# Kernel tuning notes

Measured on AMD Instinct MI355X. Metric: run time of the kernel, lower is better.

Reference implementation:

```python
import jax, jax.numpy as jnp
import numpy as np

# ranges from init_kwargs
T2P_RANGE = (1.0, 500.0)
B1_RANGE = (0.2, 1.6)

NX, NY = 256, 256
NUM_T2S, NUM_B1S, ETL = 100, 30, 16


def _nan_to_num0(x):
    # torch.nan_to_num(x, nan=0.0, posinf=0.0); inputs here are non-negative so
    # neginf never occurs, but we zero it too for safety.
    return jnp.nan_to_num(x, nan=0.0, posinf=0.0, neginf=0.0)


def setup_inputs() -> dict:
    key = jax.random.key(0)
    k1, k2, k3 = jax.random.split(key, 3)
    slice_signal = jax.random.uniform(k1, (NX, NY, ETL), dtype=jnp.float32)
    db_mag = jax.random.uniform(k2, (NUM_T2S, NUM_B1S, ETL), dtype=jnp.float32)
    db_t2s_ms = jnp.linspace(1.0, 1000.0, NUM_T2S, dtype=jnp.float32)
    db_b1s = jnp.linspace(0.2, 1.6, NUM_B1S, dtype=jnp.float32)
    delta_t_t2p_ms = 9.0 * jnp.arange(1, ETL + 1, dtype=jnp.float32)  # echo times
    estimates = jax.random.uniform(k3, (2, NX, NY), dtype=jnp.float32)
    return {
        "slice_signal": slice_signal,
        "db_mag": db_mag,
        "db_t2s_ms": db_t2s_ms,
        "db_b1s": db_b1s,
        "delta_t_t2p_ms": delta_t_t2p_ms,
        "estimates": estimates,
    }


def reference(slice_signal, db_mag, db_t2s_ms, db_b1s, delta_t_t2p_ms, estimates):
    etl = slice_signal.shape[-1]
    sig = _nan_to_num0(slice_signal / jnp.linalg.norm(slice_signal, axis=-1, keepdims=True))
    sig = sig.reshape(-1, etl)  # (P, etl)

    # b1 map from estimates[1], scaled to b1_range
    b1 = B1_RANGE[0] + (B1_RANGE[1] - B1_RANGE[0]) * estimates[1]  # (nx, ny)
    # TV term: torch.gradient default == numpy.gradient (central diff interior,
    # one-sided edges)
    g0, g1 = jnp.gradient(b1)
    f_2 = jnp.sum(jnp.abs(g0) + jnp.abs(g1))

    # nearest-neighbor B1 dictionary lookup (non-differentiable gather)
    b1_flat = b1.reshape(-1)  # (P,)
    b1_idx = jnp.argmin((b1_flat[:, None] - db_b1s[None, :]) ** 2, axis=-1)  # (P,)
    db = db_mag[:, b1_idx]  # (T2, P, etl)

    # eta = exp(-dt / t2p), t2p from estimates[0] scaled to t2p_range
    t2p = T2P_RANGE[0] + (T2P_RANGE[1] - T2P_RANGE[0]) * estimates[0].reshape(-1)  # (P,)
    eta = jnp.exp(-delta_t_t2p_ms[None, :] / t2p[:, None])  # (P, etl)

    s_db = db * eta[None]  # (T2, P, etl)
    s_db = _nan_to_num0(s_db / jnp.linalg.norm(s_db, axis=-1, keepdims=True))

    l2_min = jnp.linalg.norm(s_db - sig[None], axis=-1)  # (T2, P)
    f_1 = jnp.sum(jnp.linalg.norm(l2_min, axis=-1))  # sum over T2 of per-T2 norms over pixels
    return f_1 + f_2
```

## Files before the change

### kernel.cpp

```cpp
#include <hip/hip_runtime.h>
#include <math.h>

constexpr int NXc = 256, NYc = 256, ETLc = 16, NTc = 100, NBc = 30;
constexpr int NPIX = NXc * NYc;
constexpr int TCHUNK = 13;
constexpr int NCHUNK = 8;
constexpr int RSTRIDE = 20;


__global__ __launch_bounds__(256) void k_main(
    const float* __restrict__ sig,
    const float* __restrict__ db_mag,
    const float* __restrict__ dtt,
    const float* __restrict__ est,
    float* __restrict__ ws_f1,
    float* __restrict__ ws_f2)
{
    const int tid    = threadIdx.x;
    const int pixblk = blockIdx.x & 255;
    const int tchunk = blockIdx.x >> 8;
    const int p = (pixblk << 8) | tid;
    const int x = p >> 8;
    const int y = p & 255;
    const int t0 = tchunk * TCHUNK;

    alignas(16) __shared__ float lds[TCHUNK * NBc * RSTRIDE];
    __shared__ float s_part[TCHUNK * 4];
    __shared__ float s_f2[4];

    const int tcnt = (NTc - t0 < TCHUNK) ? (NTc - t0) : TCHUNK;
    const int nf4  = tcnt * 120;
    const float4* gsrc = reinterpret_cast<const float4*>(db_mag + (size_t)t0 * (NBc * ETLc));
    for (int i = tid; i < nf4; i += 256) {
        const int ttl = i / 120;
        const int rem = i - ttl * 120;
        const int jbl = rem >> 2;
        const int k   = rem & 3;
        float4 v = gsrc[i];
        *reinterpret_cast<float4*>(&lds[ttl * (NBc * RSTRIDE) + jbl * RSTRIDE + k * 4]) = v;
    }

    const float4* sp = reinterpret_cast<const float4*>(sig + (size_t)p * ETLc);
    float s[16];
    {
        float4 a = sp[0], b = sp[1], c = sp[2], d = sp[3];
        s[0]=a.x; s[1]=a.y; s[2]=a.z;  s[3]=a.w;
        s[4]=b.x; s[5]=b.y; s[6]=b.z;  s[7]=b.w;
        s[8]=c.x; s[9]=c.y; s[10]=c.z; s[11]=c.w;
        s[12]=d.x; s[13]=d.y; s[14]=d.z; s[15]=d.w;
    }
    float snrm2 = 0.f;
#pragma unroll
    for (int e = 0; e < 16; ++e) snrm2 = fmaf(s[e], s[e], snrm2);
    const float sig2  = (snrm2 > 0.f) ? 1.0f : 0.0f;
    const float srinv = (snrm2 > 0.f) ? __builtin_amdgcn_rsqf(snrm2) : 0.0f;
    float sgn[16];
#pragma unroll
    for (int e = 0; e < 16; ++e) sgn[e] = s[e] * srinv;

    const float est0 = est[p];
    const float t2p  = 1.0f + 499.0f * est0;
    const float nrcp = -__builtin_amdgcn_rcpf(t2p);
    float eta[16];
#pragma unroll
    for (int e = 0; e < 16; ++e) eta[e] = __expf(dtt[e] * nrcp);

    const float est1 = est[NPIX + p];
    float kf = roundf(est1 * 29.0f);
    kf = fminf(fmaxf(kf, 0.0f), 29.0f);
    const int jb = (int)kf;

    const int wid = tid >> 6, lane = tid & 63;
    __syncthreads();

#pragma unroll 2
    for (int tt = 0; tt < TCHUNK; ++tt) {
        float r = 0.f;
        if (t0 + tt < NTc) {
            const float4* lp = reinterpret_cast<const float4*>(
                &lds[tt * (NBc * RSTRIDE) + jb * RSTRIDE]);
            float4 a = lp[0], b = lp[1], c = lp[2], d = lp[3];
            float dbr[16];
            dbr[0]=a.x; dbr[1]=a.y; dbr[2]=a.z;  dbr[3]=a.w;
            dbr[4]=b.x; dbr[5]=b.y; dbr[6]=b.z;  dbr[7]=b.w;
            dbr[8]=c.x; dbr[9]=c.y; dbr[10]=c.z; dbr[11]=c.w;
            dbr[12]=d.x; dbr[13]=d.y; dbr[14]=d.z; dbr[15]=d.w;

            float nrm2 = 0.f, dotv = 0.f;
#pragma unroll
            for (int e = 0; e < 16; ++e) {
                float v = dbr[e] * eta[e];
                nrm2 = fmaf(v, v, nrm2);
                dotv = fmaf(v, sgn[e], dotv);
            }
            float l2sq;
            if (nrm2 > 0.f) l2sq = sig2 + 1.0f - 2.0f * dotv * __builtin_amdgcn_rsqf(nrm2);
            else            l2sq = sig2;
            r = (l2sq < 0.f) ? 0.f : l2sq;
        }
#pragma unroll
        for (int m = 32; m; m >>= 1) r += __shfl_xor(r, m, 64);
        if (lane == 0) s_part[tt * 4 + wid] = r;
    }
    __syncthreads();
    if (tid < TCHUNK && t0 + tid < NTc) {
        float bsum = s_part[tid*4+0] + s_part[tid*4+1] + s_part[tid*4+2] + s_part[tid*4+3];
        ws_f1[(size_t)(t0 + tid) * 256 + pixblk] = bsum;
    }

    if (tchunk == 0) {
        const float* e1 = est + NPIX;
        const float b1 = 0.2f + 1.4f * est1;
        float g0, g1;
        {
            float c = b1;
            if (x == 0)            g0 = (0.2f + 1.4f * e1[p + 256]) - c;
            else if (x == NXc - 1) g0 = c - (0.2f + 1.4f * e1[p - 256]);
            else                   g0 = 0.5f * ((0.2f + 1.4f * e1[p + 256]) - (0.2f + 1.4f * e1[p - 256]));
            if (y == 0)            g1 = (0.2f + 1.4f * e1[p + 1]) - c;
            else if (y == NYc - 1) g1 = c - (0.2f + 1.4f * e1[p - 1]);
            else                   g1 = 0.5f * ((0.2f + 1.4f * e1[p + 1]) - (0.2f + 1.4f * e1[p - 1]));
        }
        float r = fabsf(g0) + fabsf(g1);
#pragma unroll
        for (int m = 32; m; m >>= 1) r += __shfl_xor(r, m, 64);
        if (lane == 0) s_f2[wid] = r;
        __syncthreads();
        if (tid == 0) ws_f2[pixblk] = s_f2[0] + s_f2[1] + s_f2[2] + s_f2[3];
    }
}

__global__ __launch_bounds__(512) void k_final(
    const float* __restrict__ ws_f1,
    const float* __restrict__ ws_f2,
    float* __restrict__ out)
{
    const int tid = threadIdx.x;
    const int t = tid >> 2, g = tid & 3;
    float sum = 0.f;
    if (t < NTc) {
        const float4* p4 = reinterpret_cast<const float4*>(ws_f1 + (size_t)t * 256 + g * 64);
#pragma unroll
        for (int i = 0; i < 16; ++i) { float4 v = p4[i]; sum += (v.x + v.y) + (v.z + v.w); }
    }
    sum += __shfl_xor(sum, 1, 64);
    sum += __shfl_xor(sum, 2, 64);

    __shared__ float s_sq[128];
    if (tid < 128) s_sq[tid] = 0.f;
    __syncthreads();
    if (g == 0 && t < NTc) s_sq[t] = sqrtf(sum);
    __syncthreads();

    if (tid < 64) {
        float v = s_sq[tid] + s_sq[tid + 64];
        v += (ws_f2[tid] + ws_f2[tid + 64]) + (ws_f2[tid + 128] + ws_f2[tid + 192]);
#pragma unroll
        for (int m = 32; m; m >>= 1) v += __shfl_xor(v, m, 64);
        if (tid == 0) out[0] = v;
    }
}

extern "C" void kernel_launch(void* const* d_in, const int* in_sizes, int n_in,
                              void* d_out, int out_size, void* d_ws, size_t ws_size,
                              hipStream_t stream) {
    const float* sig    = (const float*)d_in[0];
    const float* db_mag = (const float*)d_in[1];
    const float* dtt    = (const float*)d_in[4];
    const float* est    = (const float*)d_in[5];
    float* out = (float*)d_out;

    float* ws_f1 = (float*)d_ws;
    float* ws_f2 = ws_f1 + (size_t)NTc * 256;

    k_main <<<dim3(256 * NCHUNK), dim3(256), 0, stream>>>(sig, db_mag, dtt, est, ws_f1, ws_f2);
    k_final<<<dim3(1),            dim3(512), 0, stream>>>(ws_f1, ws_f2, out);
}
```

Baseline: 27.83 us.

## Sort pixels by B1 bin within block to reduce LDS bank conflicts

Each block now builds a histogram of B1 dictionary indices in shared memory, prefix-sums it, and reorders its threads so threads with the same B1 bin sit next to each other. Because each wavefront then reads fewer distinct LDS rows, the per-T2 dictionary loads should hit fewer bank conflicts and broadcast more. The cost is extra shared-memory atomics, three more barriers, and uncoalesced gathered signal loads. The TV-gradient computation moves ahead of the main loop.

```diff
diff --git a/kernel.cpp b/kernel.cpp
--- a/kernel.cpp
+++ b/kernel.cpp
@@ -23,10 +23,16 @@
     const int x = p >> 8;
     const int y = p & 255;
     const int t0 = tchunk * TCHUNK;
+    const int wid = tid >> 6, lane = tid & 63;
 
     alignas(16) __shared__ float lds[TCHUNK * NBc * RSTRIDE];
     __shared__ float s_part[TCHUNK * 4];
     __shared__ float s_f2[4];
+    __shared__ int s_hist[NBc];
+    __shared__ int s_base[NBc];
+    __shared__ unsigned char s_ord[256];
+
+    if (tid < NBc) s_hist[tid] = 0;
 
     const int tcnt = (NTc - t0 < TCHUNK) ? (NTc - t0) : TCHUNK;
     const int nf4  = tcnt * 120;
@@ -40,7 +46,48 @@
         *reinterpret_cast<float4*>(&lds[ttl * (NBc * RSTRIDE) + jbl * RSTRIDE + k * 4]) = v;
     }
 
-    const float4* sp = reinterpret_cast<const float4*>(sig + (size_t)p * ETLc);
+    const float est1_own = est[NPIX + p];
+    float kfo = roundf(est1_own * 29.0f);
+    kfo = fminf(fmaxf(kfo, 0.0f), 29.0f);
+    const int jb_own = (int)kfo;
+
+    __syncthreads();
+    atomicAdd(&s_hist[jb_own], 1);
+
+    float f2r = 0.f;
+    if (tchunk == 0) {
+        const float* e1 = est + NPIX;
+        const float c = 0.2f + 1.4f * est1_own;
+        float g0, g1;
+        if (x == 0)            g0 = (0.2f + 1.4f * e1[p + 256]) - c;
+        else if (x == NXc - 1) g0 = c - (0.2f + 1.4f * e1[p - 256]);
+        else                   g0 = 0.5f * ((0.2f + 1.4f * e1[p + 256]) - (0.2f + 1.4f * e1[p - 256]));
+        if (y == 0)            g1 = (0.2f + 1.4f * e1[p + 1]) - c;
+        else if (y == NYc - 1) g1 = c - (0.2f + 1.4f * e1[p - 1]);
+        else                   g1 = 0.5f * ((0.2f + 1.4f * e1[p + 1]) - (0.2f + 1.4f * e1[p - 1]));
+        f2r = fabsf(g0) + fabsf(g1);
+#pragma unroll
+        for (int m = 32; m; m >>= 1) f2r += __shfl_xor(f2r, m, 64);
+        if (lane == 0) s_f2[wid] = f2r;
+    }
+
+    __syncthreads();
+    if (tid == 0) {
+        int a = 0;
+#pragma unroll
+        for (int j = 0; j < NBc; ++j) { s_base[j] = a; a += s_hist[j]; }
+        if (tchunk == 0) ws_f2[pixblk] = s_f2[0] + s_f2[1] + s_f2[2] + s_f2[3];
+    }
+    __syncthreads();
+    {
+        const int rank = atomicAdd(&s_base[jb_own], 1);
+        s_ord[rank] = (unsigned char)tid;
+    }
+    __syncthreads();
+
+    const int q = (pixblk << 8) | (int)s_ord[tid];
+
+    const float4* sp = reinterpret_cast<const float4*>(sig + (size_t)q * ETLc);
     float s[16];
     {
         float4 a = sp[0], b = sp[1], c = sp[2], d = sp[3];
@@ -58,20 +105,17 @@
 #pragma unroll
     for (int e = 0; e < 16; ++e) sgn[e] = s[e] * srinv;
 
-    const float est0 = est[p];
+    const float est0 = est[q];
     const float t2p  = 1.0f + 499.0f * est0;
     const float nrcp = -__builtin_amdgcn_rcpf(t2p);
     float eta[16];
 #pragma unroll
     for (int e = 0; e < 16; ++e) eta[e] = __expf(dtt[e] * nrcp);
 
-    const float est1 = est[NPIX + p];
+    const float est1 = est[NPIX + q];
     float kf = roundf(est1 * 29.0f);
     kf = fminf(fmaxf(kf, 0.0f), 29.0f);
     const int jb = (int)kf;
-
-    const int wid = tid >> 6, lane = tid & 63;
-    __syncthreads();
 
 #pragma unroll 2
     for (int tt = 0; tt < TCHUNK; ++tt) {
@@ -107,27 +151,6 @@
         float bsum = s_part[tid*4+0] + s_part[tid*4+1] + s_part[tid*4+2] + s_part[tid*4+3];
         ws_f1[(size_t)(t0 + tid) * 256 + pixblk] = bsum;
     }
-
-    if (tchunk == 0) {
-        const float* e1 = est + NPIX;
-        const float b1 = 0.2f + 1.4f * est1;
-        float g0, g1;
-        {
-            float c = b1;
-            if (x == 0)            g0 = (0.2f + 1.4f * e1[p + 256]) - c;
-            else if (x == NXc - 1) g0 = c - (0.2f + 1.4f * e1[p - 256]);
-            else                   g0 = 0.5f * ((0.2f + 1.4f * e1[p + 256]) - (0.2f + 1.4f * e1[p - 256]));
-            if (y == 0)            g1 = (0.2f + 1.4f * e1[p + 1]) - c;
-            else if (y == NYc - 1) g1 = c - (0.2f + 1.4f * e1[p - 1]);
-            else                   g1 = 0.5f * ((0.2f + 1.4f * e1[p + 1]) - (0.2f + 1.4f * e1[p - 1]));
-        }
-        float r = fabsf(g0) + fabsf(g1);
-#pragma unroll
-        for (int m = 32; m; m >>= 1) r += __shfl_xor(r, m, 64);
-        if (lane == 0) s_f2[wid] = r;
-        __syncthreads();
-        if (tid == 0) ws_f2[pixblk] = s_f2[0] + s_f2[1] + s_f2[2] + s_f2[3];
-    }
 }
 
 __global__ __launch_bounds__(512) void k_final(
```

Result: no change. 28.32 us (+1.8%).
